# Kernel optimization log

Measured on AMD Instinct MI355X. Metric: run time of the kernel, lower is better.

## Reference

```python
import jax, jax.numpy as jnp
import numpy as np

B, L, S, D_MODEL, H = 4, 2048, 2048, 512, 8
E = D_MODEL // H  # head dim = 64


def setup_inputs() -> dict:
    key = jax.random.key(0)
    ks = jax.random.split(key, 11)
    s = 1.0 / np.sqrt(D_MODEL)
    return {
        "queries": jax.random.normal(ks[0], (B, L, D_MODEL), jnp.float32),
        "keys": jax.random.normal(ks[1], (B, S, D_MODEL), jnp.float32),
        "values": jax.random.normal(ks[2], (B, S, D_MODEL), jnp.float32),
        "Wq": jax.random.normal(ks[3], (D_MODEL, D_MODEL), jnp.float32) * s,
        "bq": jnp.zeros((D_MODEL,), jnp.float32),
        "Wk": jax.random.normal(ks[4], (D_MODEL, D_MODEL), jnp.float32) * s,
        "bk": jnp.zeros((D_MODEL,), jnp.float32),
        "Wv": jax.random.normal(ks[5], (D_MODEL, D_MODEL), jnp.float32) * s,
        "bv": jnp.zeros((D_MODEL,), jnp.float32),
        "Wo": jax.random.normal(ks[6], (D_MODEL, D_MODEL), jnp.float32) * s,
        "bo": jnp.zeros((D_MODEL,), jnp.float32),
    }


def reference(queries, keys, values, Wq, bq, Wk, bk, Wv, bv, Wo, bo):
    # QKV projections, then split heads: [B, T, H, E]
    q = (queries @ Wq + bq).reshape(B, L, H, E)
    k = (keys @ Wk + bk).reshape(B, S, H, E)
    v = (values @ Wv + bv).reshape(B, S, H, E)
    scale = 1.0 / np.sqrt(E)
    # Naive full attention: materialized [B, H, L, S] scores (as in original)
    scores = jnp.einsum('blhe,bshe->bhls', q, k)
    A = jax.nn.softmax(scale * scores, axis=-1)  # dropout = identity at eval
    out = jnp.einsum('bhls,bshd->blhd', A, v).reshape(B, L, H * E)
    return out @ Wo + bo
```

## Files before the change

kernel.cpp:

```cpp
#include <hip/hip_runtime.h>
#include <hip/hip_bf16.h>


typedef __attribute__((ext_vector_type(8))) short bf8_t;
typedef __attribute__((ext_vector_type(4))) float f4_t;
typedef __attribute__((ext_vector_type(16))) float f16_t;
typedef __attribute__((ext_vector_type(4))) unsigned int u32x4;

#define D_MODEL 512
#define HEADS 8
#define EDIM 64
#define LSEQ 2048
#define NBATCH 4
#define MTOT (NBATCH * LSEQ)
#define N4 (MTOT * D_MODEL / 4)

static __device__ __forceinline__ unsigned short f2bf(float f) {
  union { float f; unsigned int u; } x;
  x.f = f;
  unsigned int u = x.u;
  u += 0x7FFFu + ((u >> 16) & 1u);
  return (unsigned short)(u >> 16);
}

static __device__ __forceinline__ unsigned int pack2bf(float a, float b) {
  union { __hip_bfloat162 h; unsigned int u; } c;
  c.h.x = __float2bfloat16(a);
  c.h.y = __float2bfloat16(b);
  return c.u;
}

#define GLOAD_LDS(gptr, lptr)                                                        \
  __builtin_amdgcn_global_load_lds((const __attribute__((address_space(1))) void*)(gptr), \
                                   (__attribute__((address_space(3))) void*)(lptr), 16, 0, 0)

__global__ void prep_all(const float* __restrict__ q, const float* __restrict__ k,
                         const float* __restrict__ v,
                         const float* __restrict__ Wq, const float* __restrict__ Wk,
                         const float* __restrict__ Wv, const float* __restrict__ Wo,
                         unsigned short* __restrict__ Xq, unsigned short* __restrict__ Xk,
                         unsigned short* __restrict__ Xv,
                         unsigned short* __restrict__ Wqt, unsigned short* __restrict__ Wkt,
                         unsigned short* __restrict__ Wvt, unsigned short* __restrict__ Wot) {
  __shared__ float tile[64][65];
  const int blk = blockIdx.x;
  if (blk < 12288) {
    int i = blk * 256 + threadIdx.x;
    int which = i >> 20;
    int idx = i & (N4 - 1);
    const float* in = (which == 0) ? q : (which == 1) ? k : v;
    unsigned short* out = (which == 0) ? Xq : (which == 1) ? Xk : Xv;
    float4 x = ((const float4*)in)[idx];
    ushort4 o;
    o.x = f2bf(x.x); o.y = f2bf(x.y); o.z = f2bf(x.z); o.w = f2bf(x.w);
    ((ushort4*)out)[idx] = o;
  } else {
    const int b = blk - 12288;
    const int which = b >> 6;
    const int b2 = b & 63;
    const int k0 = (b2 >> 3) * 64, n0 = (b2 & 7) * 64;
    const float* W = (which == 0) ? Wq : (which == 1) ? Wk : (which == 2) ? Wv : Wo;
    unsigned short* Wt = (which == 0) ? Wqt : (which == 1) ? Wkt : (which == 2) ? Wvt : Wot;
    const int tx = threadIdx.x & 63;
    const int ty = threadIdx.x >> 6;
#pragma unroll
    for (int i = 0; i < 64; i += 4)
      tile[i + ty][tx] = W[(size_t)(k0 + i + ty) * D_MODEL + n0 + tx];
    __syncthreads();
#pragma unroll
    for (int i = 0; i < 64; i += 4)
      Wt[(size_t)(n0 + i + ty) * D_MODEL + k0 + tx] = f2bf(tile[tx][i + ty]);
  }
}

__device__ __forceinline__ void stage_a(const unsigned short* __restrict__ A,
                                        unsigned short* lA, int m0, int k0) {
  const int t = threadIdx.x;
  int rowA = t >> 2, cbA = (t & 3) * 16;
  GLOAD_LDS((const char*)(A + (size_t)(m0 + rowA) * D_MODEL + k0) + cbA, (char*)lA + t * 16);
}
__device__ __forceinline__ void stage_b(const unsigned short* __restrict__ Bt,
                                        unsigned short* lB, int n0, int k0) {
  const int t = threadIdx.x;
#pragma unroll
  for (int ii = 0; ii < 2; ++ii) {
    int c = t + ii * 256;
    int rowB = c >> 2, cbB = (c & 3) * 16;
    GLOAD_LDS((const char*)(Bt + (size_t)(n0 + rowB) * D_MODEL + k0) + cbB, (char*)lB + c * 16);
  }
}

__device__ __forceinline__ void gemm_core(const unsigned short* __restrict__ A,
                                          const unsigned short* __restrict__ Bt,
                                          unsigned short* __restrict__ lAv,
                                          unsigned short* __restrict__ lBv,
                                          f4_t (&acc)[2][4], int m0, int n0) {
  const int t = threadIdx.x;
  const int lane = t & 63;
  const int w = t >> 6;
  const int wr = w >> 1, wc = w & 1;
  const int r = lane & 15, g = lane >> 4;
  const int ASZ = 64 * 32, BSZ = 128 * 32;

  stage_a(A, lAv, m0, 0);
  stage_b(Bt, lBv, n0, 0);
  __syncthreads();

  int cur = 0;
  const int NK = D_MODEL / 32;
  for (int ks = 0; ks < NK; ++ks) {
    if (ks + 1 < NK) {
      const int kn = (ks + 1) * 32;
      stage_a(A, lAv + (cur ^ 1) * ASZ, m0, kn);
      stage_b(Bt, lBv + (cur ^ 1) * BSZ, n0, kn);
    }

    bf8_t af[2], bfv[4];
    const unsigned short* lA = lAv + cur * ASZ;
#pragma unroll
    for (int mi = 0; mi < 2; ++mi)
      af[mi] = *(const bf8_t*)(lA + (wr * 32 + mi * 16 + r) * 32 + g * 8);
    const unsigned short* lB = lBv + cur * BSZ;
#pragma unroll
    for (int ni = 0; ni < 4; ++ni)
      bfv[ni] = *(const bf8_t*)(lB + (wc * 64 + ni * 16 + r) * 32 + g * 8);
#pragma unroll
    for (int mi = 0; mi < 2; ++mi)
#pragma unroll
      for (int ni = 0; ni < 4; ++ni)
        acc[mi][ni] = __builtin_amdgcn_mfma_f32_16x16x32_bf16(af[mi], bfv[ni], acc[mi][ni], 0, 0, 0);
    __syncthreads();
    cur ^= 1;
  }
}

#define QSCALE 0.18033688011112042f
__global__ __launch_bounds__(256, 6) void qkv_gemm(
    const unsigned short* __restrict__ Xq, const unsigned short* __restrict__ Xk,
    const unsigned short* __restrict__ Xv,
    const unsigned short* __restrict__ Wqt, const unsigned short* __restrict__ Wkt,
    const unsigned short* __restrict__ Wvt,
    const float* __restrict__ bq, const float* __restrict__ bk, const float* __restrict__ bv,
    unsigned short* __restrict__ Qh, unsigned short* __restrict__ Kh,
    unsigned short* __restrict__ Vt) {
  __shared__ alignas(16) unsigned short lA[2][64 * 32];
  __shared__ alignas(16) unsigned short lB[2][128 * 32];
  const int p = blockIdx.x;
  const int res = p & 7, q = p >> 3;
  const int xx = q & 3;
  const int grp = res + ((q >> 2) << 3);
  const int z = grp >> 7;
  const int y = grp & 127;
  const int n0 = xx * 128, m0 = y * 64;

  const unsigned short* A  = (z == 0) ? Xq : (z == 1) ? Xk : Xv;
  const unsigned short* Bt = (z == 0) ? Wqt : (z == 1) ? Wkt : Wvt;
  const float* bias        = (z == 0) ? bq : (z == 1) ? bk : bv;

  f4_t acc[2][4] = {};
  gemm_core(A, Bt, &lA[0][0], &lB[0][0], acc, m0, n0);

  const int lane = threadIdx.x & 63;
  const int w = threadIdx.x >> 6;
  const int wr = w >> 1, wc = w & 1;
  const int r = lane & 15, g = lane >> 4;
#pragma unroll
  for (int mi = 0; mi < 2; ++mi)
#pragma unroll
    for (int ni = 0; ni < 4; ++ni) {
      const int coln = n0 + wc * 64 + ni * 16 + r;
      const float bv_ = bias[coln];
      const int h = coln >> 6, e = coln & 63;
#pragma unroll
      for (int j = 0; j < 4; ++j) {
        const int rowm = m0 + wr * 32 + mi * 16 + g * 4 + j;
        const int b = rowm >> 11, li = rowm & 2047;
        float v = acc[mi][ni][j] + bv_;
        if (z == 0) {
          v *= QSCALE;
          Qh[(((size_t)(b * HEADS + h) * LSEQ + li) << 6) + e] = f2bf(v);
        } else if (z == 1) {
          Kh[(((size_t)(b * HEADS + h) * LSEQ + li) << 6) + e] = f2bf(v);
        } else {
          const int bb = (li >> 2) & 3;
          const int bs = ((bb & 1) << 1) | (bb >> 1);
          const int lp = (li & ~15) | (bs << 2) | (li & 3);
          Vt[(((size_t)(b * HEADS + h) * EDIM + e) << 11) + lp] = f2bf(v);
        }
      }
    }
}

__global__ __launch_bounds__(256, 6) void o_gemm(const unsigned short* __restrict__ A,
                                                 const unsigned short* __restrict__ Bt,
                                                 const float* __restrict__ bias,
                                                 float* __restrict__ Cout) {
  __shared__ alignas(16) unsigned short lA[2][64 * 32];
  __shared__ alignas(16) unsigned short lB[2][128 * 32];
  const int p = blockIdx.x;
  const int res = p & 7, q = p >> 3;
  const int xx = q & 3;
  const int grp = res + ((q >> 2) << 3);
  const int n0 = xx * 128, m0 = grp * 64;

  f4_t acc[2][4] = {};
  gemm_core(A, Bt, &lA[0][0], &lB[0][0], acc, m0, n0);

  const int lane = threadIdx.x & 63;
  const int w = threadIdx.x >> 6;
  const int wr = w >> 1, wc = w & 1;
  const int r = lane & 15, g = lane >> 4;
#pragma unroll
  for (int mi = 0; mi < 2; ++mi)
#pragma unroll
    for (int ni = 0; ni < 4; ++ni) {
      const int coln = n0 + wc * 64 + ni * 16 + r;
      const float bv_ = bias[coln];
#pragma unroll
      for (int j = 0; j < 4; ++j) {
        const int rowm = m0 + wr * 32 + mi * 16 + g * 4 + j;
        Cout[(size_t)rowm * D_MODEL + coln] = acc[mi][ni][j] + bv_;
      }
    }
}

#define XSTR 68

__device__ __forceinline__ void stage_tile(const unsigned short* __restrict__ Kbase,
                                           const unsigned short* __restrict__ Vbase,
                                           unsigned short* ldsK, unsigned short* ldsV,
                                           int s0, int tg) {
#pragma unroll
  for (int ii = 0; ii < 2; ++ii) {
    int c = tg + ii * 256;
    int row = c >> 3, col = c & 7;
    int colp = col ^ (row & 7);
    GLOAD_LDS((const char*)(Kbase + (size_t)(s0 + row) * EDIM + colp * 8),
              (char*)ldsK + c * 16);
    GLOAD_LDS((const char*)(Vbase + (size_t)row * LSEQ + s0 + colp * 8),
              (char*)ldsV + c * 16);
  }
}

__global__ __launch_bounds__(512, 4) void flash_attn(const unsigned short* __restrict__ Qh,
                                                     const unsigned short* __restrict__ Kh,
                                                     const unsigned short* __restrict__ Vt,
                                                     unsigned short* __restrict__ Ao) {
  __shared__ alignas(16) unsigned short stg[2][2][2][64 * 64];

  const int t = threadIdx.x;
  const int lane = t & 63;
  const int w = t >> 6;
  const int wg = w >> 2;
  const int wq = w & 3;
  const int tg = t & 255;
  const int qn = lane & 31;
  const int hi = lane >> 5;
  const int p = blockIdx.x;
  const int xcd = p & 7, jj = p >> 3;
  const int bh = xcd * 4 + (jj >> 4);
  const int qblk = jj & 15;
  const int q0 = qblk * 128 + wq * 32;
  const int sbase = wg * (LSEQ / 2);

  bf8_t qf[4];
#pragma unroll
  for (int kst = 0; kst < 4; ++kst)
    qf[kst] = *(const bf8_t*)(Qh + ((size_t)bh * LSEQ + q0 + qn) * EDIM + kst * 16 + hi * 8);

  float l_lane = 0.f;
  f16_t oacc[2];
#pragma unroll
  for (int eh = 0; eh < 2; ++eh)
#pragma unroll
    for (int r = 0; r < 16; ++r) oacc[eh][r] = 0.f;

  f16_t kZero;
#pragma unroll
  for (int r = 0; r < 16; ++r) kZero[r] = 0.f;

  const unsigned short* Kbase = Kh + (size_t)bh * LSEQ * EDIM;
  const unsigned short* Vbase = Vt + (size_t)bh * EDIM * LSEQ;

  stage_tile(Kbase, Vbase, stg[wg][0][0], stg[wg][0][1], sbase, tg);
  __syncthreads();

  const int NT = LSEQ / 2 / 64;
#pragma unroll 2
  for (int kt = 0; kt < NT; ++kt) {
    const int cur = kt & 1;
    if (kt + 1 < NT)
      stage_tile(Kbase, Vbase, stg[wg][cur ^ 1][0], stg[wg][cur ^ 1][1],
                 sbase + (kt + 1) * 64, tg);

    const unsigned short* lsK = stg[wg][cur][0];
    const unsigned short* lsV = stg[wg][cur][1];

    bf8_t kf[2][4];
#pragma unroll
    for (int sh = 0; sh < 2; ++sh)
#pragma unroll
      for (int kst = 0; kst < 4; ++kst) {
        const int row = 32 * sh + qn;
        const int ch = (2 * kst + hi) ^ (row & 7);
        kf[sh][kst] = *(const bf8_t*)(&lsK[row * 64 + ch * 8]);
      }
    f16_t sacc[2];
#pragma unroll
    for (int sh = 0; sh < 2; ++sh) {
      sacc[sh] = __builtin_amdgcn_mfma_f32_32x32x16_bf16(kf[sh][0], qf[0], kZero, 0, 0, 0);
#pragma unroll
      for (int kst = 1; kst < 4; ++kst)
        sacc[sh] = __builtin_amdgcn_mfma_f32_32x32x16_bf16(kf[sh][kst], qf[kst], sacc[sh], 0, 0, 0);
    }

    unsigned int pk[16];
#pragma unroll
    for (int sh = 0; sh < 2; ++sh)
#pragma unroll
      for (int i = 0; i < 8; ++i) {
        const float a = __builtin_amdgcn_exp2f(sacc[sh][2 * i]);
        const float b = __builtin_amdgcn_exp2f(sacc[sh][2 * i + 1]);
        l_lane += a + b;
        pk[sh * 8 + i] = pack2bf(a, b);
      }

    bf8_t pvb[4];
#pragma unroll
    for (int t2 = 0; t2 < 4; ++t2) {
      union { u32x4 u; bf8_t b; } pb;
      pb.u[0] = pk[4 * t2 + 0];
      pb.u[1] = pk[4 * t2 + 1];
      pb.u[2] = pk[4 * t2 + 2];
      pb.u[3] = pk[4 * t2 + 3];
      pvb[t2] = pb.b;
    }

#pragma unroll
    for (int eh = 0; eh < 2; ++eh)
#pragma unroll
      for (int t2 = 0; t2 < 4; ++t2) {
        const int row = 32 * eh + qn;
        const int ch = (2 * t2 + hi) ^ (row & 7);
        const bf8_t vf = *(const bf8_t*)(&lsV[row * 64 + ch * 8]);
        oacc[eh] = __builtin_amdgcn_mfma_f32_32x32x16_bf16(vf, pvb[t2], oacc[eh], 0, 0, 0);
      }

    __syncthreads();
  }

  const float l_own = l_lane + __shfl_xor(l_lane, 32);
  float* xO = (float*)&stg[0][0][0][0];
  float* xL = xO + 128 * XSTR;

  if (wg == 1) {
#pragma unroll
    for (int eh = 0; eh < 2; ++eh)
#pragma unroll
      for (int k = 0; k < 4; ++k) {
        float4 v4;
        v4.x = oacc[eh][4 * k + 0]; v4.y = oacc[eh][4 * k + 1];
        v4.z = oacc[eh][4 * k + 2]; v4.w = oacc[eh][4 * k + 3];
        *(float4*)(xO + (wq * 32 + qn) * XSTR + 32 * eh + 8 * k + 4 * hi) = v4;
      }
    if (hi == 0) xL[wq * 32 + qn] = l_own;
  }
  __syncthreads();

  if (wg == 0) {
    const float inv = 1.f / (l_own + xL[wq * 32 + qn]);
    const int b = bh >> 3, h = bh & 7;
#pragma unroll
    for (int eh = 0; eh < 2; ++eh)
#pragma unroll
      for (int k = 0; k < 4; ++k) {
        const float4 v4 = *(const float4*)(xO + (wq * 32 + qn) * XSTR + 32 * eh + 8 * k + 4 * hi);
        ushort4 ov;
        ov.x = f2bf((oacc[eh][4 * k + 0] + v4.x) * inv);
        ov.y = f2bf((oacc[eh][4 * k + 1] + v4.y) * inv);
        ov.z = f2bf((oacc[eh][4 * k + 2] + v4.z) * inv);
        ov.w = f2bf((oacc[eh][4 * k + 3] + v4.w) * inv);
        const int e = 32 * eh + 8 * k + 4 * hi;
        *(ushort4*)(Ao + ((size_t)(b * LSEQ + q0 + qn)) * D_MODEL + h * EDIM + e) = ov;
      }
  }
}

extern "C" void kernel_launch(void* const* d_in, const int* in_sizes, int n_in,
                              void* d_out, int out_size, void* d_ws, size_t ws_size,
                              hipStream_t stream) {
  const float* queries = (const float*)d_in[0];
  const float* keys    = (const float*)d_in[1];
  const float* values  = (const float*)d_in[2];
  const float* Wq = (const float*)d_in[3];
  const float* bq = (const float*)d_in[4];
  const float* Wk = (const float*)d_in[5];
  const float* bk = (const float*)d_in[6];
  const float* Wv = (const float*)d_in[7];
  const float* bv = (const float*)d_in[8];
  const float* Wo = (const float*)d_in[9];
  const float* bo = (const float*)d_in[10];

  char* ws = (char*)d_ws;
  const size_t XSZ = (size_t)MTOT * D_MODEL * 2;
  unsigned short* Xq  = (unsigned short*)(ws + 0 * XSZ);
  unsigned short* Xk  = (unsigned short*)(ws + 1 * XSZ);
  unsigned short* Xv  = (unsigned short*)(ws + 2 * XSZ);
  unsigned short* Qh  = (unsigned short*)(ws + 3 * XSZ);
  unsigned short* Kh  = (unsigned short*)(ws + 4 * XSZ);
  unsigned short* Vt  = (unsigned short*)(ws + 5 * XSZ);
  unsigned short* Ao  = (unsigned short*)(ws + 6 * XSZ);
  unsigned short* Wqt = (unsigned short*)(ws + 7 * XSZ);
  unsigned short* Wkt = Wqt + 512 * 512;
  unsigned short* Wvt = Wkt + 512 * 512;
  unsigned short* Wot = Wvt + 512 * 512;

  prep_all<<<12544, 256, 0, stream>>>(queries, keys, values, Wq, Wk, Wv, Wo,
                                      Xq, Xk, Xv, Wqt, Wkt, Wvt, Wot);

  qkv_gemm<<<1536, 256, 0, stream>>>(
      Xq, Xk, Xv, Wqt, Wkt, Wvt, bq, bk, bv, Qh, Kh, Vt);

  flash_attn<<<512, 512, 0, stream>>>(Qh, Kh, Vt, Ao);

  o_gemm<<<512, 256, 0, stream>>>(Ao, Wot, bo, (float*)d_out);
}
```

Measured before the change: 102.9 us.

## Prefetch K/V tiles two iterations ahead with split staging and vmcnt waits

Splits K and V staging into separate functions and restructures the double-buffered loop to prefetch tiles two iterations ahead. K is reloaded into the current buffer right after its fragments are read, and V right after the PV MFMAs. Partial vmcnt waits replace full __syncthreads, so global-to-LDS loads overlap more compute. This adds extra barriers per iteration and relies on correct manual vmcnt counting.

```diff
diff --git a/kernel.cpp b/kernel.cpp
--- a/kernel.cpp
+++ b/kernel.cpp
@@ -226,10 +226,8 @@
 
 #define XSTR 68
 
-__device__ __forceinline__ void stage_tile(const unsigned short* __restrict__ Kbase,
-                                           const unsigned short* __restrict__ Vbase,
-                                           unsigned short* ldsK, unsigned short* ldsV,
-                                           int s0, int tg) {
+__device__ __forceinline__ void stage_K(const unsigned short* __restrict__ Kbase,
+                                        unsigned short* ldsK, int s0, int tg) {
 #pragma unroll
   for (int ii = 0; ii < 2; ++ii) {
     int c = tg + ii * 256;
@@ -237,6 +235,15 @@
     int colp = col ^ (row & 7);
     GLOAD_LDS((const char*)(Kbase + (size_t)(s0 + row) * EDIM + colp * 8),
               (char*)ldsK + c * 16);
+  }
+}
+__device__ __forceinline__ void stage_V(const unsigned short* __restrict__ Vbase,
+                                        unsigned short* ldsV, int s0, int tg) {
+#pragma unroll
+  for (int ii = 0; ii < 2; ++ii) {
+    int c = tg + ii * 256;
+    int row = c >> 3, col = c & 7;
+    int colp = col ^ (row & 7);
     GLOAD_LDS((const char*)(Vbase + (size_t)row * LSEQ + s0 + colp * 8),
               (char*)ldsV + c * 16);
   }
@@ -282,17 +289,18 @@
   const unsigned short* Kbase = Kh + (size_t)bh * LSEQ * EDIM;
   const unsigned short* Vbase = Vt + (size_t)bh * EDIM * LSEQ;
 
-  stage_tile(Kbase, Vbase, stg[wg][0][0], stg[wg][0][1], sbase, tg);
-  __syncthreads();
+  stage_K(Kbase, stg[wg][0][0], sbase, tg);
+  stage_V(Vbase, stg[wg][0][1], sbase, tg);
+  stage_K(Kbase, stg[wg][1][0], sbase + 64, tg);
+  stage_V(Vbase, stg[wg][1][1], sbase + 64, tg);
+  asm volatile("s_waitcnt vmcnt(4)" ::: "memory");
+  __builtin_amdgcn_s_barrier();
+  __builtin_amdgcn_sched_barrier(0);
 
   const int NT = LSEQ / 2 / 64;
 #pragma unroll 2
   for (int kt = 0; kt < NT; ++kt) {
     const int cur = kt & 1;
-    if (kt + 1 < NT)
-      stage_tile(Kbase, Vbase, stg[wg][cur ^ 1][0], stg[wg][cur ^ 1][1],
-                 sbase + (kt + 1) * 64, tg);
-
     const unsigned short* lsK = stg[wg][cur][0];
     const unsigned short* lsV = stg[wg][cur][1];
 
@@ -305,6 +313,12 @@
         const int ch = (2 * kst + hi) ^ (row & 7);
         kf[sh][kst] = *(const bf8_t*)(&lsK[row * 64 + ch * 8]);
       }
+    asm volatile("s_waitcnt lgkmcnt(0)" ::: "memory");
+    __builtin_amdgcn_sched_barrier(0);
+    __builtin_amdgcn_s_barrier();
+    __builtin_amdgcn_sched_barrier(0);
+    if (kt + 2 < NT) stage_K(Kbase, stg[wg][cur][0], sbase + (kt + 2) * 64, tg);
+
     f16_t sacc[2];
 #pragma unroll
     for (int sh = 0; sh < 2; ++sh) {
@@ -345,9 +359,22 @@
         const bf8_t vf = *(const bf8_t*)(&lsV[row * 64 + ch * 8]);
         oacc[eh] = __builtin_amdgcn_mfma_f32_32x32x16_bf16(vf, pvb[t2], oacc[eh], 0, 0, 0);
       }
-
-    __syncthreads();
-  }
+    asm volatile("s_waitcnt lgkmcnt(0)" ::: "memory");
+    __builtin_amdgcn_sched_barrier(0);
+    __builtin_amdgcn_s_barrier();
+    __builtin_amdgcn_sched_barrier(0);
+    if (kt + 2 < NT) stage_V(Vbase, stg[wg][cur][1], sbase + (kt + 2) * 64, tg);
+
+    if (kt + 2 < NT) {
+      asm volatile("s_waitcnt vmcnt(4)" ::: "memory");
+    } else if (kt + 1 < NT) {
+      asm volatile("s_waitcnt vmcnt(0)" ::: "memory");
+    }
+    __builtin_amdgcn_s_barrier();
+    __builtin_amdgcn_sched_barrier(0);
+  }
+
+  __syncthreads();
 
   const float l_own = l_lane + __shfl_xor(l_lane, 32);
   float* xO = (float*)&stg[0][0][0][0];
```

New measurement: 162.6 us. 58.0% more time.

## Enlarge flash-attention blocks to 1024 threads with triple-buffered K/V staging

Applied to the files above, without the earlier changes.

Doubles the flash attention block to 16 waves covering 256 queries, so each K/V tile staged in LDS is shared by twice as many query rows. It also moves from double to triple buffering, prefetching two tiles ahead, and swaps __syncthreads for manual vmcnt waits plus raw barriers. The aim is to cut redundant global K/V traffic and hide load latency. In exchange it raises LDS use to 96KB per block and halves the grid to 256 blocks, which may lower occupancy and fill the GPU less evenly.

```diff
diff --git a/kernel.cpp b/kernel.cpp
--- a/kernel.cpp
+++ b/kernel.cpp
@@ -226,41 +226,40 @@
 
 #define XSTR 68
 
-__device__ __forceinline__ void stage_tile(const unsigned short* __restrict__ Kbase,
-                                           const unsigned short* __restrict__ Vbase,
-                                           unsigned short* ldsK, unsigned short* ldsV,
-                                           int s0, int tg) {
-#pragma unroll
-  for (int ii = 0; ii < 2; ++ii) {
-    int c = tg + ii * 256;
-    int row = c >> 3, col = c & 7;
-    int colp = col ^ (row & 7);
-    GLOAD_LDS((const char*)(Kbase + (size_t)(s0 + row) * EDIM + colp * 8),
-              (char*)ldsK + c * 16);
-    GLOAD_LDS((const char*)(Vbase + (size_t)row * LSEQ + s0 + colp * 8),
-              (char*)ldsV + c * 16);
-  }
-}
-
-__global__ __launch_bounds__(512, 4) void flash_attn(const unsigned short* __restrict__ Qh,
-                                                     const unsigned short* __restrict__ Kh,
-                                                     const unsigned short* __restrict__ Vt,
-                                                     unsigned short* __restrict__ Ao) {
-  __shared__ alignas(16) unsigned short stg[2][2][2][64 * 64];
+__device__ __forceinline__ void stage_K1(const unsigned short* __restrict__ Kbase,
+                                         unsigned short* ldsK, int s0, int tg) {
+  int row = tg >> 3, col = tg & 7;
+  int colp = col ^ (row & 7);
+  GLOAD_LDS((const char*)(Kbase + (size_t)(s0 + row) * EDIM + colp * 8),
+            (char*)ldsK + tg * 16);
+}
+__device__ __forceinline__ void stage_V1(const unsigned short* __restrict__ Vbase,
+                                         unsigned short* ldsV, int s0, int tg) {
+  int row = tg >> 3, col = tg & 7;
+  int colp = col ^ (row & 7);
+  GLOAD_LDS((const char*)(Vbase + (size_t)row * LSEQ + s0 + colp * 8),
+            (char*)ldsV + tg * 16);
+}
+
+__global__ __launch_bounds__(1024, 4) void flash_attn(const unsigned short* __restrict__ Qh,
+                                                      const unsigned short* __restrict__ Kh,
+                                                      const unsigned short* __restrict__ Vt,
+                                                      unsigned short* __restrict__ Ao) {
+  __shared__ alignas(16) unsigned short stg[2][3][2][64 * 64];
 
   const int t = threadIdx.x;
   const int lane = t & 63;
   const int w = t >> 6;
-  const int wg = w >> 2;
-  const int wq = w & 3;
-  const int tg = t & 255;
+  const int wg = w >> 3;
+  const int wq = w & 7;
+  const int tg = t & 511;
   const int qn = lane & 31;
   const int hi = lane >> 5;
   const int p = blockIdx.x;
   const int xcd = p & 7, jj = p >> 3;
-  const int bh = xcd * 4 + (jj >> 4);
-  const int qblk = jj & 15;
-  const int q0 = qblk * 128 + wq * 32;
+  const int bh = xcd * 4 + (jj >> 3);
+  const int qblk = jj & 7;
+  const int q0 = qblk * 256 + wq * 32;
   const int sbase = wg * (LSEQ / 2);
 
   bf8_t qf[4];
@@ -282,19 +281,26 @@
   const unsigned short* Kbase = Kh + (size_t)bh * LSEQ * EDIM;
   const unsigned short* Vbase = Vt + (size_t)bh * EDIM * LSEQ;
 
-  stage_tile(Kbase, Vbase, stg[wg][0][0], stg[wg][0][1], sbase, tg);
-  __syncthreads();
+  unsigned short *rK = &stg[wg][0][0][0], *rV = &stg[wg][0][1][0];
+  unsigned short *nK = &stg[wg][1][0][0], *nV = &stg[wg][1][1][0];
+  unsigned short *sK = &stg[wg][2][0][0], *sV = &stg[wg][2][1][0];
+
+  stage_K1(Kbase, rK, sbase, tg);
+  stage_V1(Vbase, rV, sbase, tg);
+  stage_K1(Kbase, nK, sbase + 64, tg);
+  stage_V1(Vbase, nV, sbase + 64, tg);
+  asm volatile("s_waitcnt vmcnt(2)" ::: "memory");
+  __builtin_amdgcn_s_barrier();
+  __builtin_amdgcn_sched_barrier(0);
 
   const int NT = LSEQ / 2 / 64;
-#pragma unroll 2
   for (int kt = 0; kt < NT; ++kt) {
-    const int cur = kt & 1;
-    if (kt + 1 < NT)
-      stage_tile(Kbase, Vbase, stg[wg][cur ^ 1][0], stg[wg][cur ^ 1][1],
-                 sbase + (kt + 1) * 64, tg);
-
-    const unsigned short* lsK = stg[wg][cur][0];
-    const unsigned short* lsV = stg[wg][cur][1];
+    if (kt + 2 < NT) {
+      stage_K1(Kbase, sK, sbase + (kt + 2) * 64, tg);
+      stage_V1(Vbase, sV, sbase + (kt + 2) * 64, tg);
+    }
+    const unsigned short* lsK = rK;
+    const unsigned short* lsV = rV;
 
     bf8_t kf[2][4];
 #pragma unroll
@@ -346,12 +352,27 @@
         oacc[eh] = __builtin_amdgcn_mfma_f32_32x32x16_bf16(vf, pvb[t2], oacc[eh], 0, 0, 0);
       }
 
-    __syncthreads();
-  }
+    if (kt + 2 < NT) {
+      asm volatile("s_waitcnt vmcnt(2) lgkmcnt(0)" ::: "memory");
+    } else if (kt + 1 < NT) {
+      asm volatile("s_waitcnt vmcnt(0) lgkmcnt(0)" ::: "memory");
+    } else {
+      asm volatile("s_waitcnt lgkmcnt(0)" ::: "memory");
+    }
+    __builtin_amdgcn_s_barrier();
+    __builtin_amdgcn_sched_barrier(0);
+
+    unsigned short* tK = rK; unsigned short* tV = rV;
+    rK = nK; rV = nV;
+    nK = sK; nV = sV;
+    sK = tK; sV = tV;
+  }
+
+  __syncthreads();
 
   const float l_own = l_lane + __shfl_xor(l_lane, 32);
   float* xO = (float*)&stg[0][0][0][0];
-  float* xL = xO + 128 * XSTR;
+  float* xL = xO + 256 * XSTR;
 
   if (wg == 1) {
 #pragma unroll
@@ -421,7 +442,7 @@
   qkv_gemm<<<1536, 256, 0, stream>>>(
       Xq, Xk, Xv, Wqt, Wkt, Wvt, bq, bk, bv, Qh, Kh, Vt);
 
-  flash_attn<<<512, 512, 0, stream>>>(Qh, Kh, Vt, Ao);
+  flash_attn<<<256, 1024, 0, stream>>>(Qh, Kh, Vt, Ao);
 
   o_gemm<<<512, 256, 0, stream>>>(Ao, Wot, bo, (float*)d_out);
 }
```

Result: no change. 101.1 us (-1.8%).
